# Performance work log

Hardware: AMD Instinct MI355X
Metric: run time of the kernel (lower is better)

The kernel has to match this reference:

```python
import jax, jax.numpy as jnp
import numpy as np

D_MODEL = 4096
NUM_EXPERTS = 64
TOP_K = 2


def setup_inputs() -> dict:
    key = jax.random.key(0)
    kx, kw, kb = jax.random.split(key, 3)
    x = jax.random.normal(kx, (4, 4096, D_MODEL), dtype=jnp.float32)
    # nn.Linear default init ~ U(-1/sqrt(fan_in), 1/sqrt(fan_in))
    bound = 1.0 / np.sqrt(D_MODEL)
    W = jax.random.uniform(kw, (D_MODEL, NUM_EXPERTS), minval=-bound, maxval=bound, dtype=jnp.float32)
    b = jax.random.uniform(kb, (NUM_EXPERTS,), minval=-bound, maxval=bound, dtype=jnp.float32)
    return {"x": x, "W": W, "b": b}


def reference(x, W, b):
    # gate: [B,S,D] @ [D,E] -> [B,S,E]
    logits = jnp.einsum('bsd,de->bse', x, W) + b
    probs = jax.nn.softmax(logits, axis=-1)
    topk_probs, topk_indices = jax.lax.top_k(probs, TOP_K)
    topk_probs = topk_probs / (jnp.sum(topk_probs, axis=-1, keepdims=True) + 1e-9)
    return probs, topk_probs, topk_indices
```

## Files before the change

kernel.cpp:

```cpp
#include <hip/hip_runtime.h>

#define D_MODEL 4096
#define NEXP    64
#define NTOK    16384
#define NKS     128

typedef _Float16 half8 __attribute__((ext_vector_type(8)));
typedef float    f32x4 __attribute__((ext_vector_type(4)));

__device__ __forceinline__ void split8(float4 a, float4 b, half8& hi, half8& lo) {
    auto h0 = __builtin_amdgcn_cvt_pkrtz(a.x, a.y);
    auto h1 = __builtin_amdgcn_cvt_pkrtz(a.z, a.w);
    auto h2 = __builtin_amdgcn_cvt_pkrtz(b.x, b.y);
    auto h3 = __builtin_amdgcn_cvt_pkrtz(b.z, b.w);
    hi[0] = static_cast<_Float16>(h0[0]); hi[1] = static_cast<_Float16>(h0[1]);
    hi[2] = static_cast<_Float16>(h1[0]); hi[3] = static_cast<_Float16>(h1[1]);
    hi[4] = static_cast<_Float16>(h2[0]); hi[5] = static_cast<_Float16>(h2[1]);
    hi[6] = static_cast<_Float16>(h3[0]); hi[7] = static_cast<_Float16>(h3[1]);
    float r0 = a.x - (float)h0[0], r1 = a.y - (float)h0[1];
    float r2 = a.z - (float)h1[0], r3 = a.w - (float)h1[1];
    float r4 = b.x - (float)h2[0], r5 = b.y - (float)h2[1];
    float r6 = b.z - (float)h3[0], r7 = b.w - (float)h3[1];
    auto l0 = __builtin_amdgcn_cvt_pkrtz(r0, r1);
    auto l1 = __builtin_amdgcn_cvt_pkrtz(r2, r3);
    auto l2 = __builtin_amdgcn_cvt_pkrtz(r4, r5);
    auto l3 = __builtin_amdgcn_cvt_pkrtz(r6, r7);
    lo[0] = static_cast<_Float16>(l0[0]); lo[1] = static_cast<_Float16>(l0[1]);
    lo[2] = static_cast<_Float16>(l1[0]); lo[3] = static_cast<_Float16>(l1[1]);
    lo[4] = static_cast<_Float16>(l2[0]); lo[5] = static_cast<_Float16>(l2[1]);
    lo[6] = static_cast<_Float16>(l3[0]); lo[7] = static_cast<_Float16>(l3[1]);
}

__global__ __launch_bounds__(256) void prep_w(const float* __restrict__ W,
                                              half8* __restrict__ ws) {
    const int gid  = blockIdx.x * 256 + threadIdx.x;
    const int lane = gid & 63;
    const int fp   = gid >> 6;
    const int t    = fp & 3;
    const int ks   = fp >> 2;
    const int e    = 16 * t + (lane & 15);
    const int k0   = ks * 32 + (lane >> 4) * 8;
    float4 a, b;
    a.x = W[(size_t)(k0 + 0) * NEXP + e];
    a.y = W[(size_t)(k0 + 1) * NEXP + e];
    a.z = W[(size_t)(k0 + 2) * NEXP + e];
    a.w = W[(size_t)(k0 + 3) * NEXP + e];
    b.x = W[(size_t)(k0 + 4) * NEXP + e];
    b.y = W[(size_t)(k0 + 5) * NEXP + e];
    b.z = W[(size_t)(k0 + 6) * NEXP + e];
    b.w = W[(size_t)(k0 + 7) * NEXP + e];
    half8 hi, lo;
    split8(a, b, hi, lo);
    ws[(size_t)(fp * 2 + 0) * 64 + lane] = hi;
    ws[(size_t)(fp * 2 + 1) * 64 + lane] = lo;
}

__global__ __launch_bounds__(256, 1) void router_mfma(
    const float* __restrict__ x, const int4* __restrict__ wf,
    const float* __restrict__ b, float* __restrict__ out)
{
    __shared__ float ls[4][16][68];
    const int tid  = threadIdx.x;
    const int lane = tid & 63;
    const int wv   = tid >> 6;
    const int tok0 = blockIdx.x * 64 + wv * 16;
    const int m    = lane & 15;
    const int q    = lane >> 4;
    const float* __restrict__ xrow = x + (size_t)(tok0 + m) * D_MODEL + q * 8;

    f32x4 acc[4] = {};

    float4 xc[2][2], xn[2][2];
    int4   wc[2][4][2], wn[2][4][2];

    auto ldx = [&](int c, float4 dst[2][2]) {
#pragma unroll
        for (int s = 0; s < 2; s++) {
            const float* p = xrow + (c * 2 + s) * 32;
            dst[s][0] = *(const float4*)p;
            dst[s][1] = *(const float4*)(p + 4);
        }
    };
    auto ldw = [&](int c, int4 dst[2][4][2]) {
#pragma unroll
        for (int s = 0; s < 2; s++) {
            const int ks = c * 2 + s;
#pragma unroll
            for (int t = 0; t < 4; t++) {
                const int fi = (ks * 4 + t) * 2;
                dst[s][t][0] = wf[(size_t)fi * 64 + lane];
                dst[s][t][1] = wf[(size_t)(fi + 1) * 64 + lane];
            }
        }
    };

    ldx(0, xc);
    ldw(0, wc);
#pragma unroll 1
    for (int c = 0; c < 64; c++) {
        const int nc = (c < 63) ? c + 1 : 0;
        ldx(nc, xn);
        ldw(nc, wn);
#pragma unroll
        for (int s = 0; s < 2; s++) {
            half8 ahi, alo;
            split8(xc[s][0], xc[s][1], ahi, alo);
#pragma unroll
            for (int t = 0; t < 4; t++) {
                half8 bhi = __builtin_bit_cast(half8, wc[s][t][0]);
                half8 blo = __builtin_bit_cast(half8, wc[s][t][1]);
                acc[t] = __builtin_amdgcn_mfma_f32_16x16x32_f16(ahi, bhi, acc[t], 0, 0, 0);
                acc[t] = __builtin_amdgcn_mfma_f32_16x16x32_f16(ahi, blo, acc[t], 0, 0, 0);
                acc[t] = __builtin_amdgcn_mfma_f32_16x16x32_f16(alo, bhi, acc[t], 0, 0, 0);
            }
        }
#pragma unroll
        for (int s = 0; s < 2; s++) {
            xc[s][0] = xn[s][0]; xc[s][1] = xn[s][1];
#pragma unroll
            for (int t = 0; t < 4; t++) {
                wc[s][t][0] = wn[s][t][0];
                wc[s][t][1] = wn[s][t][1];
            }
        }
    }

#pragma unroll
    for (int t = 0; t < 4; t++)
#pragma unroll
        for (int r = 0; r < 4; r++)
            ls[wv][q * 4 + r][t * 16 + m] = acc[t][r];

    const float bias = b[lane];
    float* __restrict__ probs_out = out;
    float* __restrict__ top_out   = out + (size_t)NTOK * NEXP;
    float* __restrict__ idx_out   = top_out + (size_t)NTOK * 2;

#pragma unroll 1
    for (int r2 = 0; r2 < 16; r2++) {
        const int token = tok0 + r2;
        float logit = ls[wv][r2][lane] + bias;

        float mx = logit;
#pragma unroll
        for (int off = 32; off; off >>= 1) mx = fmaxf(mx, __shfl_xor(mx, off, 64));
        float ex = expf(logit - mx);
        float s = ex;
#pragma unroll
        for (int off = 32; off; off >>= 1) s += __shfl_xor(s, off, 64);
        float p = ex / s;
        probs_out[(size_t)token * NEXP + lane] = p;

        float v = p; int idx = lane;
#pragma unroll
        for (int off = 32; off; off >>= 1) {
            float ov = __shfl_xor(v, off, 64);
            int   oi = __shfl_xor(idx, off, 64);
            if (ov > v || (ov == v && oi < idx)) { v = ov; idx = oi; }
        }
        const float v1 = v; const int i1 = idx;
        v = (lane == i1) ? -1.0f : p; idx = lane;
#pragma unroll
        for (int off = 32; off; off >>= 1) {
            float ov = __shfl_xor(v, off, 64);
            int   oi = __shfl_xor(idx, off, 64);
            if (ov > v || (ov == v && oi < idx)) { v = ov; idx = oi; }
        }
        const float v2 = v; const int i2 = idx;

        if (lane == 0) {
            const float dnm = v1 + v2 + 1e-9f;
            top_out[(size_t)token * 2 + 0] = v1 / dnm;
            top_out[(size_t)token * 2 + 1] = v2 / dnm;
            idx_out[(size_t)token * 2 + 0] = (float)i1;
            idx_out[(size_t)token * 2 + 1] = (float)i2;
        }
    }
}

#define BK  128
#define BKP (BK + 4)
__device__ __forceinline__ float rl(float v, int l) {
    return __int_as_float(__builtin_amdgcn_readlane(__float_as_int(v), l));
}
__global__ __launch_bounds__(128) void router_fallback(
    const float* __restrict__ x, const float* __restrict__ W,
    const float* __restrict__ b, float* __restrict__ out)
{
    __shared__ float wt[NEXP * BKP];
    const int tid  = threadIdx.x;
    const int lane = tid & 63;
    const int wv   = __builtin_amdgcn_readfirstlane(tid >> 6);
    const int tok0 = blockIdx.x * 16 + wv * 8;
    const float* __restrict__ xw = x + (size_t)tok0 * D_MODEL;

    float2 xcur[8], xnxt[8];
#pragma unroll
    for (int t = 0; t < 8; t++)
        xcur[t] = *(const float2*)(xw + (size_t)t * D_MODEL + 2 * lane);
    float accm[8];
#pragma unroll
    for (int t = 0; t < 8; t++) accm[t] = 0.f;

    for (int c = 0; c < D_MODEL / BK; c++) {
        const int k0 = c * BK;
        if (c + 1 < D_MODEL / BK) {
#pragma unroll
            for (int t = 0; t < 8; t++)
                xnxt[t] = *(const float2*)(xw + (size_t)t * D_MODEL + (k0 + BK) + 2 * lane);
        }
#pragma unroll
        for (int i = 0; i < 16; i++) {
            int n  = i * 128 + tid;
            int dd = n >> 4;
            int e0 = (n & 15) * 4;
            float4 v = *(const float4*)(W + (size_t)(k0 + dd) * NEXP + e0);
            wt[(e0 + 0) * BKP + dd] = v.x;
            wt[(e0 + 1) * BKP + dd] = v.y;
            wt[(e0 + 2) * BKP + dd] = v.z;
            wt[(e0 + 3) * BKP + dd] = v.w;
        }
        __syncthreads();
        float acc[8];
#pragma unroll
        for (int t = 0; t < 8; t++) acc[t] = 0.f;
        const float* wl = &wt[lane * BKP];
#pragma unroll 4
        for (int kk = 0; kk < BK; kk += 4) {
            float4 w4 = *(const float4*)(wl + kk);
            const int l0 = kk >> 1;
#pragma unroll
            for (int t = 0; t < 8; t++) {
                float a = acc[t];
                a = fmaf(rl(xcur[t].x, l0    ), w4.x, a);
                a = fmaf(rl(xcur[t].y, l0    ), w4.y, a);
                a = fmaf(rl(xcur[t].x, l0 + 1), w4.z, a);
                a = fmaf(rl(xcur[t].y, l0 + 1), w4.w, a);
                acc[t] = a;
            }
        }
#pragma unroll
        for (int t = 0; t < 8; t++) accm[t] += acc[t];
        __syncthreads();
#pragma unroll
        for (int t = 0; t < 8; t++) xcur[t] = xnxt[t];
    }

    const float bias = b[lane];
    float* __restrict__ probs_out = out;
    float* __restrict__ top_out   = out + (size_t)NTOK * NEXP;
    float* __restrict__ idx_out   = top_out + (size_t)NTOK * 2;
#pragma unroll 1
    for (int t = 0; t < 8; t++) {
        const int token = tok0 + t;
        float logit = accm[t] + bias;
        float mx = logit;
#pragma unroll
        for (int off = 32; off; off >>= 1) mx = fmaxf(mx, __shfl_xor(mx, off, 64));
        float ex = expf(logit - mx);
        float s = ex;
#pragma unroll
        for (int off = 32; off; off >>= 1) s += __shfl_xor(s, off, 64);
        float p = ex / s;
        probs_out[(size_t)token * NEXP + lane] = p;
        float v = p; int idx = lane;
#pragma unroll
        for (int off = 32; off; off >>= 1) {
            float ov = __shfl_xor(v, off, 64);
            int   oi = __shfl_xor(idx, off, 64);
            if (ov > v || (ov == v && oi < idx)) { v = ov; idx = oi; }
        }
        const float v1 = v; const int i1 = idx;
        v = (lane == i1) ? -1.0f : p; idx = lane;
#pragma unroll
        for (int off = 32; off; off >>= 1) {
            float ov = __shfl_xor(v, off, 64);
            int   oi = __shfl_xor(idx, off, 64);
            if (ov > v || (ov == v && oi < idx)) { v = ov; idx = oi; }
        }
        const float v2 = v; const int i2 = idx;
        if (lane == 0) {
            const float dnm = v1 + v2 + 1e-9f;
            top_out[(size_t)token * 2 + 0] = v1 / dnm;
            top_out[(size_t)token * 2 + 1] = v2 / dnm;
            idx_out[(size_t)token * 2 + 0] = (float)i1;
            idx_out[(size_t)token * 2 + 1] = (float)i2;
        }
    }
}

extern "C" void kernel_launch(void* const* d_in, const int* in_sizes, int n_in,
                              void* d_out, int out_size, void* d_ws, size_t ws_size,
                              hipStream_t stream) {
    const float* x = (const float*)d_in[0];
    const float* W = (const float*)d_in[1];
    const float* b = (const float*)d_in[2];
    float* out = (float*)d_out;

    const size_t need = (size_t)NKS * 4 * 2 * 64 * 16;
    if (ws_size >= need) {
        prep_w<<<128, 256, 0, stream>>>(W, (half8*)d_ws);
        router_mfma<<<256, 256, 0, stream>>>(x, (const int4*)d_ws, b, out);
    } else {
        router_fallback<<<NTOK / 16, 128, 0, stream>>>(x, W, b, out);
    }
}
```

Measured before the change: 424.2 us.

## Split expert tiles across waves and shrink blocks to 16 tokens

Each block now handles 16 tokens, and each of its four waves computes one 16-expert tile instead of all 64 experts for its own 16 tokens. The grid grows to NTOK/16 blocks, and launch bounds allow 4 blocks per CU, which aims to raise occupancy and hide memory latency in this latency-bound matmul. The register double-buffer swap is replaced by a two-stage ping-pong prefetch. The cost is that every wave in a block loads and fp16-splits the same x rows, so that work is done four times over, and a block-level sync is needed before the softmax/top-k epilogue.

```diff
diff --git a/kernel.cpp b/kernel.cpp
--- a/kernel.cpp
+++ b/kernel.cpp
@@ -4,6 +4,7 @@
 #define NEXP    64
 #define NTOK    16384
 #define NKS     128
+#define NCH     64
 
 typedef _Float16 half8 __attribute__((ext_vector_type(8)));
 typedef float    f32x4 __attribute__((ext_vector_type(4)));
@@ -55,25 +56,25 @@
     ws[(size_t)(fp * 2 + 1) * 64 + lane] = lo;
 }
 
-__global__ __launch_bounds__(256, 1) void router_mfma(
+__global__ __launch_bounds__(256, 4) void router_mfma(
     const float* __restrict__ x, const int4* __restrict__ wf,
     const float* __restrict__ b, float* __restrict__ out)
 {
-    __shared__ float ls[4][16][68];
+    __shared__ float ls[16][68];
     const int tid  = threadIdx.x;
     const int lane = tid & 63;
     const int wv   = tid >> 6;
-    const int tok0 = blockIdx.x * 64 + wv * 16;
+    const int tok0 = blockIdx.x * 16;
     const int m    = lane & 15;
     const int q    = lane >> 4;
     const float* __restrict__ xrow = x + (size_t)(tok0 + m) * D_MODEL + q * 8;
 
-    f32x4 acc[4] = {};
-
-    float4 xc[2][2], xn[2][2];
-    int4   wc[2][4][2], wn[2][4][2];
-
-    auto ldx = [&](int c, float4 dst[2][2]) {
+    f32x4 acc = {};
+
+    float4 xb[2][2][2];
+    int4   wb[2][2][2];
+
+    auto ldx = [&](int c, float4 (&dst)[2][2]) {
 #pragma unroll
         for (int s = 0; s < 2; s++) {
             const float* p = xrow + (c * 2 + s) * 32;
@@ -81,55 +82,38 @@
             dst[s][1] = *(const float4*)(p + 4);
         }
     };
-    auto ldw = [&](int c, int4 dst[2][4][2]) {
+    auto ldw = [&](int c, int4 (&dst)[2][2]) {
 #pragma unroll
         for (int s = 0; s < 2; s++) {
-            const int ks = c * 2 + s;
-#pragma unroll
-            for (int t = 0; t < 4; t++) {
-                const int fi = (ks * 4 + t) * 2;
-                dst[s][t][0] = wf[(size_t)fi * 64 + lane];
-                dst[s][t][1] = wf[(size_t)(fi + 1) * 64 + lane];
-            }
+            const int fi = ((c * 2 + s) * 4 + wv) * 2;
+            dst[s][0] = wf[(size_t)fi * 64 + lane];
+            dst[s][1] = wf[(size_t)(fi + 1) * 64 + lane];
         }
     };
 
-    ldx(0, xc);
-    ldw(0, wc);
-#pragma unroll 1
-    for (int c = 0; c < 64; c++) {
-        const int nc = (c < 63) ? c + 1 : 0;
-        ldx(nc, xn);
-        ldw(nc, wn);
+    ldx(0, xb[0]); ldw(0, wb[0]);
+    ldx(1, xb[1]); ldw(1, wb[1]);
+
+#pragma unroll 2
+    for (int c = 0; c < NCH; c++) {
+        const int p = c & 1;
 #pragma unroll
         for (int s = 0; s < 2; s++) {
             half8 ahi, alo;
-            split8(xc[s][0], xc[s][1], ahi, alo);
-#pragma unroll
-            for (int t = 0; t < 4; t++) {
-                half8 bhi = __builtin_bit_cast(half8, wc[s][t][0]);
-                half8 blo = __builtin_bit_cast(half8, wc[s][t][1]);
-                acc[t] = __builtin_amdgcn_mfma_f32_16x16x32_f16(ahi, bhi, acc[t], 0, 0, 0);
-                acc[t] = __builtin_amdgcn_mfma_f32_16x16x32_f16(ahi, blo, acc[t], 0, 0, 0);
-                acc[t] = __builtin_amdgcn_mfma_f32_16x16x32_f16(alo, bhi, acc[t], 0, 0, 0);
-            }
-        }
-#pragma unroll
-        for (int s = 0; s < 2; s++) {
-            xc[s][0] = xn[s][0]; xc[s][1] = xn[s][1];
-#pragma unroll
-            for (int t = 0; t < 4; t++) {
-                wc[s][t][0] = wn[s][t][0];
-                wc[s][t][1] = wn[s][t][1];
-            }
-        }
-    }
-
-#pragma unroll
-    for (int t = 0; t < 4; t++)
-#pragma unroll
-        for (int r = 0; r < 4; r++)
-            ls[wv][q * 4 + r][t * 16 + m] = acc[t][r];
+            split8(xb[p][s][0], xb[p][s][1], ahi, alo);
+            half8 bhi = __builtin_bit_cast(half8, wb[p][s][0]);
+            half8 blo = __builtin_bit_cast(half8, wb[p][s][1]);
+            acc = __builtin_amdgcn_mfma_f32_16x16x32_f16(ahi, bhi, acc, 0, 0, 0);
+            acc = __builtin_amdgcn_mfma_f32_16x16x32_f16(ahi, blo, acc, 0, 0, 0);
+            acc = __builtin_amdgcn_mfma_f32_16x16x32_f16(alo, bhi, acc, 0, 0, 0);
+        }
+        if (c + 2 < NCH) { ldx(c + 2, xb[p]); ldw(c + 2, wb[p]); }
+    }
+
+#pragma unroll
+    for (int r = 0; r < 4; r++)
+        ls[q * 4 + r][wv * 16 + m] = acc[r];
+    __syncthreads();
 
     const float bias = b[lane];
     float* __restrict__ probs_out = out;
@@ -137,9 +121,10 @@
     float* __restrict__ idx_out   = top_out + (size_t)NTOK * 2;
 
 #pragma unroll 1
-    for (int r2 = 0; r2 < 16; r2++) {
-        const int token = tok0 + r2;
-        float logit = ls[wv][r2][lane] + bias;
+    for (int r2 = 0; r2 < 4; r2++) {
+        const int trow  = wv * 4 + r2;
+        const int token = tok0 + trow;
+        float logit = ls[trow][lane] + bias;
 
         float mx = logit;
 #pragma unroll
@@ -300,7 +285,7 @@
     const size_t need = (size_t)NKS * 4 * 2 * 64 * 16;
     if (ws_size >= need) {
         prep_w<<<128, 256, 0, stream>>>(W, (half8*)d_ws);
-        router_mfma<<<256, 256, 0, stream>>>(x, (const int4*)d_ws, b, out);
+        router_mfma<<<NTOK / 16, 256, 0, stream>>>(x, (const int4*)d_ws, b, out);
     } else {
         router_fallback<<<NTOK / 16, 128, 0, stream>>>(x, W, b, out);
     }
```

After: 454.3 us. 7.1% more time.
